# Performance work log

Hardware: AMD Instinct MI355X
Metric: run time of the kernel (lower is better)

The kernel has to match this reference:

```python
import jax, jax.numpy as jnp
import numpy as np

B, D, C = 8192, 1024, 8  # batch, input_size, n_conditions


def setup_inputs() -> dict:
    key = jax.random.key(0)
    k1, k2, k3, k4 = jax.random.split(key, 4)
    x = jax.random.normal(k1, (B, D), dtype=jnp.float32)
    condition_ids = jax.random.randint(k2, (B,), 0, C)  # metadata[batch_key] codes
    # Per-condition Linear(D, D) weights (torch layout: [out, in]) and biases
    W = jax.random.normal(k3, (C, D, D), dtype=jnp.float32) / np.sqrt(D)
    b = jax.random.normal(k4, (C, D), dtype=jnp.float32) * 0.01
    return {"x": x, "condition_ids": condition_ids, "W": W, "b": b}


def reference(x, condition_ids, W, b):
    # Original: for each condition c, zero non-member rows of x, apply
    # Linear_c to the FULL batch, then sum partials. Because Linear is
    # affine, the summed result per row is:
    #   out[i] = W[c_i] @ x[i] + sum_c b_c
    # (each bias b_c is added to EVERY row since the Linear runs on the
    #  full masked batch). We keep the dense per-condition GEMM structure.
    onehot = jax.nn.one_hot(condition_ids, C, dtype=x.dtype)  # [B, C]
    y = jnp.einsum('bi,coi->cbo', x, W)                       # [C, B, D]
    out = jnp.einsum('cbo,bc->bo', y, onehot) + b.sum(axis=0)  # [B, D]
    return out
```

## Files before the change

kernel.cpp:

```cpp
#include <hip/hip_runtime.h>
#include <hip/hip_bf16.h>
#include <cstdint>

#define B_ROWS 8192
#define DIM    1024
#define NC     8
#define NXCD   8
#define SLOTS  16

typedef __bf16 bf16;
typedef __bf16 bf16x4 __attribute__((ext_vector_type(4)));
typedef __bf16 bf16x8 __attribute__((ext_vector_type(8)));
typedef float  f32x4  __attribute__((ext_vector_type(4)));

typedef __attribute__((address_space(3))) void* lds_vp;
typedef const __attribute__((address_space(1))) void* gbl_vp;

__global__ __launch_bounds__(1024) void route_kernel(
    const int* __restrict__ ids, const float* __restrict__ b,
    int* __restrict__ row_list, int* __restrict__ xmeta,
    float* __restrict__ bias_sum) {
    __shared__ int wtot_s[16][NC];
    __shared__ int cnt_s[NC];
    __shared__ int off_s[NC];
    __shared__ int used_s[NXCD];
    __shared__ int novf_s[NC];
    int tid = threadIdx.x, lane = tid & 63, wv = tid >> 6;
    const int per = B_ROWS / 1024;
    int base = tid * per;

    if (tid < NXCD * SLOTS) xmeta[tid * 3 + 2] = 0;

    const int4* idv = (const int4*)(ids + base);
    int4 v0 = idv[0], v1 = idv[1];
    int myid[8] = {v0.x, v0.y, v0.z, v0.w, v1.x, v1.y, v1.z, v1.w};
    unsigned long long p0 = 0, p1 = 0;
#pragma unroll
    for (int q = 0; q < 8; q++) {
        int id = myid[q];
        unsigned long long one = 1ull << ((id & 3) << 4);
        if (id < 4) p0 += one; else p1 += one;
    }
    unsigned long long i0 = p0, i1 = p1;
#pragma unroll
    for (int d = 1; d < 64; d <<= 1) {
        unsigned long long u0 = __shfl_up(i0, d, 64);
        unsigned long long u1 = __shfl_up(i1, d, 64);
        if (lane >= d) { i0 += u0; i1 += u1; }
    }
    unsigned long long e0 = i0 - p0, e1 = i1 - p1;
    unsigned long long t0 = __shfl(i0, 63, 64), t1 = __shfl(i1, 63, 64);
    if (lane == 0) {
#pragma unroll
        for (int c = 0; c < 4; c++) {
            wtot_s[wv][c]     = (int)((t0 >> (c << 4)) & 0xFFFF);
            wtot_s[wv][c + 4] = (int)((t1 >> (c << 4)) & 0xFFFF);
        }
    }
    __syncthreads();
    if (tid < NC) {
        int acc = 0;
        for (int w2 = 0; w2 < 16; w2++) { int t = wtot_s[w2][tid]; wtot_s[w2][tid] = acc; acc += t; }
        cnt_s[tid] = acc;
    }
    __syncthreads();
    if (tid < NC) {
        int acc = 0;
        for (int c2 = 0; c2 < tid; c2++) acc += cnt_s[c2];
        off_s[tid] = acc;
    }
    __syncthreads();
    if (tid < 16 * NC) wtot_s[tid >> 3][tid & 7] += off_s[tid & 7];
    __syncthreads();

    if (tid < NC) {
        int c = tid, n = cnt_s[c];
        int tc = (n + 127) >> 7;
        int prim = tc < SLOTS ? tc : SLOTS;
        for (int t = 0; t < prim; t++) {
            int* e = xmeta + (c * SLOTS + t) * 3;
            int rc = n - t * 128; if (rc > 128) rc = 128;
            e[0] = c; e[1] = off_s[c] + t * 128; e[2] = rc;
        }
        used_s[c] = prim;
        novf_s[c] = tc - prim;
    }
    {
        float s = 0.f;
#pragma unroll
        for (int c = 0; c < NC; c++) s += b[c * DIM + tid];
        bias_sum[tid] = s;
    }
    __syncthreads();

    if (tid == 0) {
        int k = 0;
        for (int c = 0; c < NC; c++) {
            for (int t = 0; t < novf_s[c]; t++) {
                for (;;) {
                    int xx = k >> 4, s = k & (SLOTS - 1); k++;
                    if (s >= used_s[xx]) {
                        int* e = xmeta + (xx * SLOTS + s) * 3;
                        int rc = cnt_s[c] - (SLOTS + t) * 128; if (rc > 128) rc = 128;
                        e[0] = c; e[1] = off_s[c] + (SLOTS + t) * 128; e[2] = rc;
                        break;
                    }
                }
            }
        }
    }
    unsigned long long r0 = 0, r1 = 0;
#pragma unroll
    for (int j = 0; j < per; j++) {
        int id = myid[j];
        int sh = (id & 3) << 4;
        unsigned long long run = (id < 4) ? r0 : r1;
        unsigned long long exc = (id < 4) ? e0 : e1;
        int p = wtot_s[wv][id] + (int)((exc >> sh) & 0xFFFF) + (int)((run >> sh) & 0xFFFF);
        row_list[p] = base + j;
        unsigned long long one = 1ull << sh;
        if (id < 4) r0 += one; else r1 += one;
    }
}

#define XF4 (B_ROWS * DIM / 4)
__global__ __launch_bounds__(1024) void cvt_kernel(
    const float* __restrict__ x, const float* __restrict__ W,
    bf16* __restrict__ xb, bf16* __restrict__ wb) {
    size_t base = (size_t)blockIdx.x * 8192 + threadIdx.x;
    const float4* src;
    bf16* dst;
    if (base < (size_t)XF4) { src = (const float4*)x; dst = xb; }
    else                    { src = (const float4*)W; dst = wb; base -= (size_t)XF4; }
    float4 v[8];
#pragma unroll
    for (int k = 0; k < 8; k++) v[k] = src[base + (size_t)k * 1024];
#pragma unroll
    for (int k = 0; k < 8; k++) {
        bf16x4 o;
        o[0] = (bf16)v[k].x; o[1] = (bf16)v[k].y;
        o[2] = (bf16)v[k].z; o[3] = (bf16)v[k].w;
        *(bf16x4*)(dst + 4 * (base + (size_t)k * 1024)) = o;
    }
}

__global__ __launch_bounds__(256, 2) void gemm_kernel(
    const bf16* __restrict__ xb, const bf16* __restrict__ wb,
    const float* __restrict__ bias_sum, const int* __restrict__ row_list,
    const int* __restrict__ xmeta, float* __restrict__ out) {
    int xcd = blockIdx.x, slot = blockIdx.y, colt = blockIdx.z;
    const int* e = xmeta + (xcd * SLOTS + slot) * 3;
    int cond = e[0], rstart = e[1], rcnt = e[2];
    if (rcnt == 0) return;
    int col0 = colt * 128;

    __shared__ bf16 lds[2][2][128 * 64];

    int tid  = threadIdx.x;
    int lane = tid & 63;
    int w    = tid >> 6;
    int wr   = w >> 1;
    int wc   = w & 1;
    int srow = lane >> 3;
    int scol = ((lane & 7) ^ srow) * 8;

    const bf16 *aS[4], *bS[4];
#pragma unroll
    for (int i = 0; i < 4; i++) {
        int tr = w * 32 + i * 8 + srow;
        int rr = (tr < rcnt) ? tr : 0;
        int grow = row_list[rstart + rr];
        aS[i] = xb + (size_t)grow * DIM + scol;
        bS[i] = wb + (size_t)cond * DIM * DIM + (size_t)(col0 + tr) * DIM + scol;
    }

    f32x4 acc[4][4];
#pragma unroll
    for (int m = 0; m < 4; m++)
#pragma unroll
        for (int n = 0; n < 4; n++) acc[m][n] = (f32x4){0.f, 0.f, 0.f, 0.f};

    int fr = lane & 15;
    int fq = lane >> 4;
    int off0 = (fq * 16) ^ ((fr & 7) << 4);
    int off1 = off0 ^ 64;

    auto stage = [&](int buf, int k0) {
#pragma unroll
        for (int i = 0; i < 4; i++) {
            __builtin_amdgcn_global_load_lds((gbl_vp)(aS[i] + k0),
                                             (lds_vp)(&lds[buf][0][(w * 32 + i * 8) * 64]),
                                             16, 0, 0);
            __builtin_amdgcn_global_load_lds((gbl_vp)(bS[i] + k0),
                                             (lds_vp)(&lds[buf][1][(w * 32 + i * 8) * 64]),
                                             16, 0, 0);
        }
    };

    stage(0, 0);
    stage(1, 64);

    const int NT = DIM / 64;
    for (int t = 0; t < NT; ++t) {
        if (t < NT - 1) asm volatile("s_waitcnt vmcnt(8)" ::: "memory");
        else            asm volatile("s_waitcnt vmcnt(0)" ::: "memory");
        __builtin_amdgcn_s_barrier();

        const char* baseA = (const char*)&lds[t & 1][0][0] + (wr * 64 + fr) * 128;
        const char* baseB = (const char*)&lds[t & 1][1][0] + (wc * 64 + fr) * 128;
#pragma unroll
        for (int kk = 0; kk < 2; ++kk) {
            int ofs = kk ? off1 : off0;
            bf16x8 af[4], bv[4];
#pragma unroll
            for (int m = 0; m < 4; m++) af[m] = *(const bf16x8*)(baseA + m * 2048 + ofs);
#pragma unroll
            for (int n = 0; n < 4; n++) bv[n] = *(const bf16x8*)(baseB + n * 2048 + ofs);
            __builtin_amdgcn_s_setprio(1);
#pragma unroll
            for (int m = 0; m < 4; m++)
#pragma unroll
                for (int n = 0; n < 4; n++)
                    acc[m][n] = __builtin_amdgcn_mfma_f32_16x16x32_bf16(
                        af[m], bv[n], acc[m][n], 0, 0, 0);
            __builtin_amdgcn_s_setprio(0);
        }

        asm volatile("s_waitcnt lgkmcnt(0)" ::: "memory");
        __builtin_amdgcn_s_barrier();
        if (t + 2 < NT) stage(t & 1, (t + 2) * 64);
    }

    float bias[4];
#pragma unroll
    for (int n = 0; n < 4; n++) bias[n] = bias_sum[col0 + wc * 64 + n * 16 + fr];
#pragma unroll
    for (int m = 0; m < 4; m++) {
#pragma unroll
        for (int i = 0; i < 4; i++) {
            int rl = wr * 64 + m * 16 + fq * 4 + i;
            if (rl < rcnt) {
                int grow = row_list[rstart + rl];
                float* op = out + (size_t)grow * DIM + col0 + wc * 64 + fr;
#pragma unroll
                for (int n = 0; n < 4; n++) op[n * 16] = acc[m][n][i] + bias[n];
            }
        }
    }
}

__global__ void naive_kernel(const float* __restrict__ x, const int* __restrict__ ids,
                             const float* __restrict__ W, const float* __restrict__ b,
                             float* __restrict__ out) {
    int row = blockIdx.x;
    int c = ids[row];
    __shared__ float xs[DIM];
    for (int i = threadIdx.x; i < DIM; i += 256) xs[i] = x[(size_t)row * DIM + i];
    __syncthreads();
    const float* Wc = W + (size_t)c * DIM * DIM;
    for (int o = threadIdx.x; o < DIM; o += 256) {
        float s = 0.f;
        const float* wrp = Wc + (size_t)o * DIM;
        for (int i = 0; i < DIM; i++) s += xs[i] * wrp[i];
        float bs = 0.f;
#pragma unroll
        for (int cc = 0; cc < NC; cc++) bs += b[cc * DIM + o];
        out[(size_t)row * DIM + o] = s + bs;
    }
}

extern "C" void kernel_launch(void* const* d_in, const int* in_sizes, int n_in,
                              void* d_out, int out_size, void* d_ws, size_t ws_size,
                              hipStream_t stream) {
    const float* x   = (const float*)d_in[0];
    const int*   ids = (const int*)d_in[1];
    const float* W   = (const float*)d_in[2];
    const float* b   = (const float*)d_in[3];
    float*       out = (float*)d_out;

    size_t xb_off   = 0;
    size_t xb_sz    = (size_t)B_ROWS * DIM * 2;
    size_t wb_off   = (xb_off + xb_sz + 255) & ~(size_t)255;
    size_t wb_sz    = (size_t)NC * DIM * DIM * 2;
    size_t bias_off = (wb_off + wb_sz + 255) & ~(size_t)255;
    size_t rl_off   = (bias_off + DIM * 4 + 255) & ~(size_t)255;
    size_t meta_off = (rl_off + B_ROWS * 4 + 255) & ~(size_t)255;
    size_t need     = meta_off + (size_t)NXCD * SLOTS * 3 * 4;

    if (ws_size < need) {
        naive_kernel<<<dim3(B_ROWS), dim3(256), 0, stream>>>(x, ids, W, b, out);
        return;
    }

    char* ws = (char*)d_ws;
    bf16*  xb       = (bf16*)(ws + xb_off);
    bf16*  wbf      = (bf16*)(ws + wb_off);
    float* bias_sum = (float*)(ws + bias_off);
    int*   row_list = (int*)(ws + rl_off);
    int*   xmeta    = (int*)(ws + meta_off);

    route_kernel<<<dim3(1), dim3(1024), 0, stream>>>(ids, b, row_list, xmeta, bias_sum);
    cvt_kernel<<<dim3(512), dim3(1024), 0, stream>>>(x, W, xb, wbf);
    gemm_kernel<<<dim3(NXCD, SLOTS, 8), dim3(256), 0, stream>>>(xb, wbf, bias_sum,
                                                                row_list, xmeta, out);
}
```

Before: 62.88 us.

## Fuse routing into conversion kernel and widen GEMM tile to 128x256

The single-block routing kernel and the fp32-to-bf16 conversion kernel are merged into one launch, with block 0 doing routing and the other blocks doing conversion. This removes one kernel launch and lets routing overlap with conversion. The GEMM moves to 512-thread blocks with a 128x256 output tile, so each loaded x tile is reused across twice as many output columns and half as many column-tile blocks are launched. The costs are more LDS per block, possibly lower occupancy, and fewer blocks to fill the device.

```diff
diff --git a/kernel.cpp b/kernel.cpp
--- a/kernel.cpp
+++ b/kernel.cpp
@@ -16,10 +16,31 @@
 typedef __attribute__((address_space(3))) void* lds_vp;
 typedef const __attribute__((address_space(1))) void* gbl_vp;
 
-__global__ __launch_bounds__(1024) void route_kernel(
+#define XF4 (B_ROWS * DIM / 4)
+__global__ __launch_bounds__(1024) void prep_kernel(
+    const float* __restrict__ x, const float* __restrict__ W,
     const int* __restrict__ ids, const float* __restrict__ b,
+    bf16* __restrict__ xb, bf16* __restrict__ wb,
     int* __restrict__ row_list, int* __restrict__ xmeta,
     float* __restrict__ bias_sum) {
+    if (blockIdx.x != 0) {
+        size_t base = (size_t)(blockIdx.x - 1) * 8192 + threadIdx.x;
+        const float4* src;
+        bf16* dst;
+        if (base < (size_t)XF4) { src = (const float4*)x; dst = xb; }
+        else                    { src = (const float4*)W; dst = wb; base -= (size_t)XF4; }
+        float4 v[8];
+#pragma unroll
+        for (int k = 0; k < 8; k++) v[k] = src[base + (size_t)k * 1024];
+#pragma unroll
+        for (int k = 0; k < 8; k++) {
+            bf16x4 o;
+            o[0] = (bf16)v[k].x; o[1] = (bf16)v[k].y;
+            o[2] = (bf16)v[k].z; o[3] = (bf16)v[k].w;
+            *(bf16x4*)(dst + 4 * (base + (size_t)k * 1024)) = o;
+        }
+        return;
+    }
     __shared__ int wtot_s[16][NC];
     __shared__ int cnt_s[NC];
     __shared__ int off_s[NC];
@@ -123,28 +144,8 @@
     }
 }
 
-#define XF4 (B_ROWS * DIM / 4)
-__global__ __launch_bounds__(1024) void cvt_kernel(
-    const float* __restrict__ x, const float* __restrict__ W,
-    bf16* __restrict__ xb, bf16* __restrict__ wb) {
-    size_t base = (size_t)blockIdx.x * 8192 + threadIdx.x;
-    const float4* src;
-    bf16* dst;
-    if (base < (size_t)XF4) { src = (const float4*)x; dst = xb; }
-    else                    { src = (const float4*)W; dst = wb; base -= (size_t)XF4; }
-    float4 v[8];
-#pragma unroll
-    for (int k = 0; k < 8; k++) v[k] = src[base + (size_t)k * 1024];
-#pragma unroll
-    for (int k = 0; k < 8; k++) {
-        bf16x4 o;
-        o[0] = (bf16)v[k].x; o[1] = (bf16)v[k].y;
-        o[2] = (bf16)v[k].z; o[3] = (bf16)v[k].w;
-        *(bf16x4*)(dst + 4 * (base + (size_t)k * 1024)) = o;
-    }
-}
-
-__global__ __launch_bounds__(256, 2) void gemm_kernel(
+#define ASZ (128 * 64)
+__global__ __launch_bounds__(512, 2) void gemm_kernel(
     const bf16* __restrict__ xb, const bf16* __restrict__ wb,
     const float* __restrict__ bias_sum, const int* __restrict__ row_list,
     const int* __restrict__ xmeta, float* __restrict__ out) {
@@ -152,26 +153,30 @@
     const int* e = xmeta + (xcd * SLOTS + slot) * 3;
     int cond = e[0], rstart = e[1], rcnt = e[2];
     if (rcnt == 0) return;
-    int col0 = colt * 128;
-
-    __shared__ bf16 lds[2][2][128 * 64];
+    int col0 = colt * 256;
+
+    __shared__ bf16 lds[2][(128 + 256) * 64];
 
     int tid  = threadIdx.x;
     int lane = tid & 63;
     int w    = tid >> 6;
-    int wr   = w >> 1;
-    int wc   = w & 1;
+    int wr   = w >> 2;
+    int wc   = w & 3;
     int srow = lane >> 3;
     int scol = ((lane & 7) ^ srow) * 8;
 
-    const bf16 *aS[4], *bS[4];
-#pragma unroll
-    for (int i = 0; i < 4; i++) {
-        int tr = w * 32 + i * 8 + srow;
+    const bf16 *aS[2], *bS[4];
+#pragma unroll
+    for (int i = 0; i < 2; i++) {
+        int tr = w * 16 + i * 8 + srow;
         int rr = (tr < rcnt) ? tr : 0;
         int grow = row_list[rstart + rr];
         aS[i] = xb + (size_t)grow * DIM + scol;
-        bS[i] = wb + (size_t)cond * DIM * DIM + (size_t)(col0 + tr) * DIM + scol;
+    }
+#pragma unroll
+    for (int i = 0; i < 4; i++) {
+        int br = w * 32 + i * 8 + srow;
+        bS[i] = wb + (size_t)cond * DIM * DIM + (size_t)(col0 + br) * DIM + scol;
     }
 
     f32x4 acc[4][4];
@@ -187,14 +192,15 @@
 
     auto stage = [&](int buf, int k0) {
 #pragma unroll
-        for (int i = 0; i < 4; i++) {
+        for (int i = 0; i < 2; i++)
             __builtin_amdgcn_global_load_lds((gbl_vp)(aS[i] + k0),
-                                             (lds_vp)(&lds[buf][0][(w * 32 + i * 8) * 64]),
+                                             (lds_vp)(&lds[buf][(w * 16 + i * 8) * 64]),
                                              16, 0, 0);
+#pragma unroll
+        for (int i = 0; i < 4; i++)
             __builtin_amdgcn_global_load_lds((gbl_vp)(bS[i] + k0),
-                                             (lds_vp)(&lds[buf][1][(w * 32 + i * 8) * 64]),
+                                             (lds_vp)(&lds[buf][ASZ + (w * 32 + i * 8) * 64]),
                                              16, 0, 0);
-        }
     };
 
     stage(0, 0);
@@ -202,12 +208,12 @@
 
     const int NT = DIM / 64;
     for (int t = 0; t < NT; ++t) {
-        if (t < NT - 1) asm volatile("s_waitcnt vmcnt(8)" ::: "memory");
+        if (t < NT - 1) asm volatile("s_waitcnt vmcnt(6)" ::: "memory");
         else            asm volatile("s_waitcnt vmcnt(0)" ::: "memory");
         __builtin_amdgcn_s_barrier();
 
-        const char* baseA = (const char*)&lds[t & 1][0][0] + (wr * 64 + fr) * 128;
-        const char* baseB = (const char*)&lds[t & 1][1][0] + (wc * 64 + fr) * 128;
+        const char* baseA = (const char*)&lds[t & 1][0] + (wr * 64 + fr) * 128;
+        const char* baseB = (const char*)&lds[t & 1][0] + ASZ * 2 + (wc * 64 + fr) * 128;
 #pragma unroll
         for (int kk = 0; kk < 2; ++kk) {
             int ofs = kk ? off1 : off0;
@@ -299,8 +305,8 @@
     int*   row_list = (int*)(ws + rl_off);
     int*   xmeta    = (int*)(ws + meta_off);
 
-    route_kernel<<<dim3(1), dim3(1024), 0, stream>>>(ids, b, row_list, xmeta, bias_sum);
-    cvt_kernel<<<dim3(512), dim3(1024), 0, stream>>>(x, W, xb, wbf);
-    gemm_kernel<<<dim3(NXCD, SLOTS, 8), dim3(256), 0, stream>>>(xb, wbf, bias_sum,
-                                                                row_list, xmeta, out);
+    prep_kernel<<<dim3(513), dim3(1024), 0, stream>>>(x, W, ids, b, xb, wbf,
+                                                      row_list, xmeta, bias_sum);
+    gemm_kernel<<<dim3(NXCD, SLOTS, DIM / 256), dim3(512), 0, stream>>>(
+        xb, wbf, bias_sum, row_list, xmeta, out);
 }
```

New measurement: 62.90 us. Within noise of the previous version (+0.0%).

## Fuse fp32-to-bf16 conversion into GEMM tile loading, drop cvt kernel

Applied to the files above, without the earlier changes.

Removes the separate conversion kernel that wrote bf16 copies of x and W to workspace. The GEMM now loads fp32 tiles through registers, converts them to bf16 and writes them to swizzled LDS. The next tile's global loads are issued before the MFMA work on the current tile. This saves a full read-write pass and a kernel launch, but each tile now reads twice as many bytes. It also gives up direct global-to-LDS loads and needs more registers, with W and x re-read in fp32 by every block.

```diff
diff --git a/kernel.cpp b/kernel.cpp
--- a/kernel.cpp
+++ b/kernel.cpp
@@ -7,14 +7,13 @@
 #define NC     8
 #define NXCD   8
 #define SLOTS  16
+#define BM     128
+#define BN     128
+#define NT     16
 
 typedef __bf16 bf16;
-typedef __bf16 bf16x4 __attribute__((ext_vector_type(4)));
 typedef __bf16 bf16x8 __attribute__((ext_vector_type(8)));
 typedef float  f32x4  __attribute__((ext_vector_type(4)));
-
-typedef __attribute__((address_space(3))) void* lds_vp;
-typedef const __attribute__((address_space(1))) void* gbl_vp;
 
 __global__ __launch_bounds__(1024) void route_kernel(
     const int* __restrict__ ids, const float* __restrict__ b,
@@ -75,12 +74,12 @@
 
     if (tid < NC) {
         int c = tid, n = cnt_s[c];
-        int tc = (n + 127) >> 7;
+        int tc = (n + BM - 1) >> 7;
         int prim = tc < SLOTS ? tc : SLOTS;
         for (int t = 0; t < prim; t++) {
             int* e = xmeta + (c * SLOTS + t) * 3;
-            int rc = n - t * 128; if (rc > 128) rc = 128;
-            e[0] = c; e[1] = off_s[c] + t * 128; e[2] = rc;
+            int rc = n - t * BM; if (rc > BM) rc = BM;
+            e[0] = c; e[1] = off_s[c] + t * BM; e[2] = rc;
         }
         used_s[c] = prim;
         novf_s[c] = tc - prim;
@@ -101,8 +100,8 @@
                     int xx = k >> 4, s = k & (SLOTS - 1); k++;
                     if (s >= used_s[xx]) {
                         int* e = xmeta + (xx * SLOTS + s) * 3;
-                        int rc = cnt_s[c] - (SLOTS + t) * 128; if (rc > 128) rc = 128;
-                        e[0] = c; e[1] = off_s[c] + (SLOTS + t) * 128; e[2] = rc;
+                        int rc = cnt_s[c] - (SLOTS + t) * BM; if (rc > BM) rc = BM;
+                        e[0] = c; e[1] = off_s[c] + (SLOTS + t) * BM; e[2] = rc;
                         break;
                     }
                 }
@@ -123,38 +122,19 @@
     }
 }
 
-#define XF4 (B_ROWS * DIM / 4)
-__global__ __launch_bounds__(1024) void cvt_kernel(
+#define BUFB 32768
+#define ABYT 16384
+__global__ __launch_bounds__(256, 2) void gemm_kernel(
     const float* __restrict__ x, const float* __restrict__ W,
-    bf16* __restrict__ xb, bf16* __restrict__ wb) {
-    size_t base = (size_t)blockIdx.x * 8192 + threadIdx.x;
-    const float4* src;
-    bf16* dst;
-    if (base < (size_t)XF4) { src = (const float4*)x; dst = xb; }
-    else                    { src = (const float4*)W; dst = wb; base -= (size_t)XF4; }
-    float4 v[8];
-#pragma unroll
-    for (int k = 0; k < 8; k++) v[k] = src[base + (size_t)k * 1024];
-#pragma unroll
-    for (int k = 0; k < 8; k++) {
-        bf16x4 o;
-        o[0] = (bf16)v[k].x; o[1] = (bf16)v[k].y;
-        o[2] = (bf16)v[k].z; o[3] = (bf16)v[k].w;
-        *(bf16x4*)(dst + 4 * (base + (size_t)k * 1024)) = o;
-    }
-}
-
-__global__ __launch_bounds__(256, 2) void gemm_kernel(
-    const bf16* __restrict__ xb, const bf16* __restrict__ wb,
     const float* __restrict__ bias_sum, const int* __restrict__ row_list,
     const int* __restrict__ xmeta, float* __restrict__ out) {
     int xcd = blockIdx.x, slot = blockIdx.y, colt = blockIdx.z;
     const int* e = xmeta + (xcd * SLOTS + slot) * 3;
     int cond = e[0], rstart = e[1], rcnt = e[2];
     if (rcnt == 0) return;
-    int col0 = colt * 128;
-
-    __shared__ bf16 lds[2][2][128 * 64];
+    int col0 = colt * BN;
+
+    __shared__ char lds[2 * BUFB];
 
     int tid  = threadIdx.x;
     int lane = tid & 63;
@@ -162,16 +142,20 @@
     int wr   = w >> 1;
     int wc   = w & 1;
     int srow = lane >> 3;
-    int scol = ((lane & 7) ^ srow) * 8;
-
-    const bf16 *aS[4], *bS[4];
+    int g    = lane & 7;
+
+    const float *aF[4], *bF[4];
+    int wofsA[4], wofsB[4];
 #pragma unroll
     for (int i = 0; i < 4; i++) {
         int tr = w * 32 + i * 8 + srow;
         int rr = (tr < rcnt) ? tr : 0;
         int grow = row_list[rstart + rr];
-        aS[i] = xb + (size_t)grow * DIM + scol;
-        bS[i] = wb + (size_t)cond * DIM * DIM + (size_t)(col0 + tr) * DIM + scol;
+        aF[i] = x + (size_t)grow * DIM + g * 8;
+        wofsA[i] = tr * 128 + ((g ^ srow) * 16);
+        int br = w * 32 + i * 8 + srow;
+        bF[i] = W + (size_t)cond * DIM * DIM + (size_t)(col0 + br) * DIM + g * 8;
+        wofsB[i] = ABYT + br * 128 + ((g ^ srow) * 16);
     }
 
     f32x4 acc[4][4];
@@ -185,37 +169,54 @@
     int off0 = (fq * 16) ^ ((fr & 7) << 4);
     int off1 = off0 ^ 64;
 
-    auto stage = [&](int buf, int k0) {
+    float4 va[4][2], vb[4][2];
+
+    auto LOAD = [&](int k0) {
 #pragma unroll
         for (int i = 0; i < 4; i++) {
-            __builtin_amdgcn_global_load_lds((gbl_vp)(aS[i] + k0),
-                                             (lds_vp)(&lds[buf][0][(w * 32 + i * 8) * 64]),
-                                             16, 0, 0);
-            __builtin_amdgcn_global_load_lds((gbl_vp)(bS[i] + k0),
-                                             (lds_vp)(&lds[buf][1][(w * 32 + i * 8) * 64]),
-                                             16, 0, 0);
+            va[i][0] = *(const float4*)(aF[i] + k0);
+            va[i][1] = *(const float4*)(aF[i] + k0 + 4);
+            vb[i][0] = *(const float4*)(bF[i] + k0);
+            vb[i][1] = *(const float4*)(bF[i] + k0 + 4);
         }
     };
-
-    stage(0, 0);
-    stage(1, 64);
-
-    const int NT = DIM / 64;
+    auto WRITE = [&](int buf) {
+#pragma unroll
+        for (int i = 0; i < 4; i++) {
+            bf16x8 oa, ob;
+            oa[0] = (bf16)va[i][0].x; oa[1] = (bf16)va[i][0].y;
+            oa[2] = (bf16)va[i][0].z; oa[3] = (bf16)va[i][0].w;
+            oa[4] = (bf16)va[i][1].x; oa[5] = (bf16)va[i][1].y;
+            oa[6] = (bf16)va[i][1].z; oa[7] = (bf16)va[i][1].w;
+            ob[0] = (bf16)vb[i][0].x; ob[1] = (bf16)vb[i][0].y;
+            ob[2] = (bf16)vb[i][0].z; ob[3] = (bf16)vb[i][0].w;
+            ob[4] = (bf16)vb[i][1].x; ob[5] = (bf16)vb[i][1].y;
+            ob[6] = (bf16)vb[i][1].z; ob[7] = (bf16)vb[i][1].w;
+            *(bf16x8*)(lds + buf * BUFB + wofsA[i]) = oa;
+            *(bf16x8*)(lds + buf * BUFB + wofsB[i]) = ob;
+        }
+    };
+
+    LOAD(0);
+    WRITE(0);
+    LOAD(64);
+    asm volatile("s_waitcnt lgkmcnt(0)" ::: "memory");
+    __builtin_amdgcn_s_barrier();
+
     for (int t = 0; t < NT; ++t) {
-        if (t < NT - 1) asm volatile("s_waitcnt vmcnt(8)" ::: "memory");
-        else            asm volatile("s_waitcnt vmcnt(0)" ::: "memory");
-        __builtin_amdgcn_s_barrier();
-
-        const char* baseA = (const char*)&lds[t & 1][0][0] + (wr * 64 + fr) * 128;
-        const char* baseB = (const char*)&lds[t & 1][1][0] + (wc * 64 + fr) * 128;
+        if (t + 1 < NT) WRITE((t + 1) & 1);
+        if (t + 2 < NT) LOAD((t + 2) * 64);
+
+        const char* bA = lds + (t & 1) * BUFB + (wr * 64 + fr) * 128;
+        const char* bB = lds + (t & 1) * BUFB + ABYT + (wc * 64 + fr) * 128;
 #pragma unroll
         for (int kk = 0; kk < 2; ++kk) {
             int ofs = kk ? off1 : off0;
             bf16x8 af[4], bv[4];
 #pragma unroll
-            for (int m = 0; m < 4; m++) af[m] = *(const bf16x8*)(baseA + m * 2048 + ofs);
-#pragma unroll
-            for (int n = 0; n < 4; n++) bv[n] = *(const bf16x8*)(baseB + n * 2048 + ofs);
+            for (int m = 0; m < 4; m++) af[m] = *(const bf16x8*)(bA + m * 2048 + ofs);
+#pragma unroll
+            for (int n = 0; n < 4; n++) bv[n] = *(const bf16x8*)(bB + n * 2048 + ofs);
             __builtin_amdgcn_s_setprio(1);
 #pragma unroll
             for (int m = 0; m < 4; m++)
@@ -228,7 +229,6 @@
 
         asm volatile("s_waitcnt lgkmcnt(0)" ::: "memory");
         __builtin_amdgcn_s_barrier();
-        if (t + 2 < NT) stage(t & 1, (t + 2) * 64);
     }
 
     float bias[4];
@@ -278,11 +278,7 @@
     const float* b   = (const float*)d_in[3];
     float*       out = (float*)d_out;
 
-    size_t xb_off   = 0;
-    size_t xb_sz    = (size_t)B_ROWS * DIM * 2;
-    size_t wb_off   = (xb_off + xb_sz + 255) & ~(size_t)255;
-    size_t wb_sz    = (size_t)NC * DIM * DIM * 2;
-    size_t bias_off = (wb_off + wb_sz + 255) & ~(size_t)255;
+    size_t bias_off = 0;
     size_t rl_off   = (bias_off + DIM * 4 + 255) & ~(size_t)255;
     size_t meta_off = (rl_off + B_ROWS * 4 + 255) & ~(size_t)255;
     size_t need     = meta_off + (size_t)NXCD * SLOTS * 3 * 4;
@@ -293,14 +289,11 @@
     }
 
     char* ws = (char*)d_ws;
-    bf16*  xb       = (bf16*)(ws + xb_off);
-    bf16*  wbf      = (bf16*)(ws + wb_off);
     float* bias_sum = (float*)(ws + bias_off);
     int*   row_list = (int*)(ws + rl_off);
     int*   xmeta    = (int*)(ws + meta_off);
 
     route_kernel<<<dim3(1), dim3(1024), 0, stream>>>(ids, b, row_list, xmeta, bias_sum);
-    cvt_kernel<<<dim3(512), dim3(1024), 0, stream>>>(x, W, xb, wbf);
-    gemm_kernel<<<dim3(NXCD, SLOTS, 8), dim3(256), 0, stream>>>(xb, wbf, bias_sum,
-                                                                row_list, xmeta, out);
-}
+    gemm_kernel<<<dim3(NXCD, SLOTS, DIM / BN), dim3(256), 0, stream>>>(
+        x, W, bias_sum, row_list, xmeta, out);
+}
```

After: 66.92 us. +6.4%, slower.

## Fuse routing, bf16 conversion and grouped GEMM into one cooperative persistent kernel

Applied to the files above, without the earlier changes.

Replaces the three launches (route, convert, GEMM) with a single cooperative kernel of 512 blocks. Block 0 does routing and the bias sum while the others convert x and W to bf16, then a grid-wide sync precedes the GEMM, where each block handles two slots. This removes launch gaps and kernel-boundary drains. It relies on all 512 blocks being co-resident, adds the cost of a grid barrier, and puts the routing on a single 256-thread block. A fallback path merges route and convert into one prep kernel followed by the GEMM.

```diff
diff --git a/kernel.cpp b/kernel.cpp
--- a/kernel.cpp
+++ b/kernel.cpp
@@ -1,12 +1,19 @@
 #include <hip/hip_runtime.h>
 #include <hip/hip_bf16.h>
+#include <hip/hip_cooperative_groups.h>
 #include <cstdint>
+
+namespace cg = cooperative_groups;
 
 #define B_ROWS 8192
 #define DIM    1024
 #define NC     8
 #define NXCD   8
 #define SLOTS  16
+#define BM     128
+#define BN     128
+#define NT     16
+#define NBLK   512
 
 typedef __bf16 bf16;
 typedef __bf16 bf16x4 __attribute__((ext_vector_type(4)));
@@ -16,10 +23,282 @@
 typedef __attribute__((address_space(3))) void* lds_vp;
 typedef const __attribute__((address_space(1))) void* gbl_vp;
 
-__global__ __launch_bounds__(1024) void route_kernel(
+#define BUFB 32768
+#define ABYT 16384
+
+__global__ __launch_bounds__(256, 2) void mega_kernel(
+    const float* __restrict__ x, const float* __restrict__ W,
     const int* __restrict__ ids, const float* __restrict__ b,
+    float* __restrict__ out, bf16* __restrict__ xb, bf16* __restrict__ wb,
+    float* __restrict__ bias_sum, int* __restrict__ row_list,
+    int* __restrict__ xmeta) {
+    __shared__ char lds[2 * BUFB];
+
+    int bid = blockIdx.x, tid = threadIdx.x;
+
+    if (bid == 0) {
+        __shared__ int wtot_s[4][NC];
+        __shared__ int cnt_s[NC];
+        __shared__ int off_s[NC];
+        __shared__ int used_s[NXCD];
+        __shared__ int novf_s[NC];
+        int lane = tid & 63, wv = tid >> 6;
+        int base = tid * 32;
+
+        if (tid < NXCD * SLOTS) xmeta[tid * 3 + 2] = 0;
+
+        unsigned long long p0 = 0, p1 = 0;
+        for (int q = 0; q < 4; q++) {
+            const int4* iv = (const int4*)(ids + base + q * 8);
+            int4 v0 = iv[0], v1 = iv[1];
+            int m[8] = {v0.x, v0.y, v0.z, v0.w, v1.x, v1.y, v1.z, v1.w};
+#pragma unroll
+            for (int j = 0; j < 8; j++) {
+                unsigned long long one = 1ull << ((m[j] & 3) << 4);
+                if (m[j] < 4) p0 += one; else p1 += one;
+            }
+        }
+        unsigned long long i0 = p0, i1 = p1;
+#pragma unroll
+        for (int d = 1; d < 64; d <<= 1) {
+            unsigned long long u0 = __shfl_up(i0, d, 64);
+            unsigned long long u1 = __shfl_up(i1, d, 64);
+            if (lane >= d) { i0 += u0; i1 += u1; }
+        }
+        unsigned long long e0 = i0 - p0, e1 = i1 - p1;
+        unsigned long long t0 = __shfl(i0, 63, 64), t1 = __shfl(i1, 63, 64);
+        if (lane == 0) {
+#pragma unroll
+            for (int c = 0; c < 4; c++) {
+                wtot_s[wv][c]     = (int)((t0 >> (c << 4)) & 0xFFFF);
+                wtot_s[wv][c + 4] = (int)((t1 >> (c << 4)) & 0xFFFF);
+            }
+        }
+        __syncthreads();
+        if (tid < NC) {
+            int acc = 0;
+            for (int w2 = 0; w2 < 4; w2++) { int t = wtot_s[w2][tid]; wtot_s[w2][tid] = acc; acc += t; }
+            cnt_s[tid] = acc;
+        }
+        __syncthreads();
+        if (tid < NC) {
+            int acc = 0;
+            for (int c2 = 0; c2 < tid; c2++) acc += cnt_s[c2];
+            off_s[tid] = acc;
+        }
+        __syncthreads();
+        if (tid < 4 * NC) wtot_s[tid >> 3][tid & 7] += off_s[tid & 7];
+        __syncthreads();
+
+        if (tid < NC) {
+            int c = tid, n = cnt_s[c];
+            int tc = (n + BM - 1) >> 7;
+            int prim = tc < SLOTS ? tc : SLOTS;
+            for (int t = 0; t < prim; t++) {
+                int* e = xmeta + (c * SLOTS + t) * 3;
+                int rc = n - t * BM; if (rc > BM) rc = BM;
+                e[0] = c; e[1] = off_s[c] + t * BM; e[2] = rc;
+            }
+            used_s[c] = prim;
+            novf_s[c] = tc - prim;
+        }
+#pragma unroll
+        for (int k = 0; k < DIM / 256; k++) {
+            int d = tid + k * 256;
+            float s = 0.f;
+#pragma unroll
+            for (int c = 0; c < NC; c++) s += b[c * DIM + d];
+            bias_sum[d] = s;
+        }
+        __syncthreads();
+        if (tid == 0) {
+            int k = 0;
+            for (int c = 0; c < NC; c++) {
+                for (int t = 0; t < novf_s[c]; t++) {
+                    for (;;) {
+                        int xx = k >> 4, s = k & (SLOTS - 1); k++;
+                        if (s >= used_s[xx]) {
+                            int* e = xmeta + (xx * SLOTS + s) * 3;
+                            int rc = cnt_s[c] - (SLOTS + t) * BM; if (rc > BM) rc = BM;
+                            e[0] = c; e[1] = off_s[c] + (SLOTS + t) * BM; e[2] = rc;
+                            break;
+                        }
+                    }
+                }
+            }
+        }
+        unsigned long long r0 = 0, r1 = 0;
+        for (int q = 0; q < 4; q++) {
+            const int4* iv = (const int4*)(ids + base + q * 8);
+            int4 v0 = iv[0], v1 = iv[1];
+            int m[8] = {v0.x, v0.y, v0.z, v0.w, v1.x, v1.y, v1.z, v1.w};
+#pragma unroll
+            for (int j = 0; j < 8; j++) {
+                int id = m[j];
+                int sh = (id & 3) << 4;
+                unsigned long long run = (id < 4) ? r0 : r1;
+                unsigned long long exc = (id < 4) ? e0 : e1;
+                int p = wtot_s[wv][id] + (int)((exc >> sh) & 0xFFFF) + (int)((run >> sh) & 0xFFFF);
+                row_list[p] = base + q * 8 + j;
+                unsigned long long one = 1ull << sh;
+                if (id < 4) r0 += one; else r1 += one;
+            }
+        }
+    } else {
+        const size_t XCHK = (size_t)B_ROWS * DIM / 8;
+        for (size_t i = (size_t)(bid - 1) * 256 + tid; i < XCHK; i += 511u * 256u) {
+            const float4* s = (const float4*)x + 2 * i;
+            float4 a = s[0], c4 = s[1];
+            bf16x8 o;
+            o[0] = (bf16)a.x;  o[1] = (bf16)a.y;  o[2] = (bf16)a.z;  o[3] = (bf16)a.w;
+            o[4] = (bf16)c4.x; o[5] = (bf16)c4.y; o[6] = (bf16)c4.z; o[7] = (bf16)c4.w;
+            *(bf16x8*)(xb + 8 * i) = o;
+        }
+        if (bid >= 8) {
+            int c = bid & 7, wi = (bid >> 3) - 1;
+            const size_t WCHK = (size_t)DIM * DIM / 8;
+            const float* Wc = W + (size_t)c * DIM * DIM;
+            bf16* wc = wb + (size_t)c * DIM * DIM;
+            for (size_t i = (size_t)wi * 256 + tid; i < WCHK; i += 63u * 256u) {
+                const float4* s = (const float4*)Wc + 2 * i;
+                float4 a = s[0], c4 = s[1];
+                bf16x8 o;
+                o[0] = (bf16)a.x;  o[1] = (bf16)a.y;  o[2] = (bf16)a.z;  o[3] = (bf16)a.w;
+                o[4] = (bf16)c4.x; o[5] = (bf16)c4.y; o[6] = (bf16)c4.z; o[7] = (bf16)c4.w;
+                *(bf16x8*)(wc + 8 * i) = o;
+            }
+        }
+    }
+
+    cg::this_grid().sync();
+
+    int xcd  = bid & 7;
+    int r    = bid >> 3;
+    int slot = r & 7;
+    int colt = r >> 3;
+    int col0 = colt * BN;
+
+    int lane = tid & 63;
+    int w    = tid >> 6;
+    int wr   = w >> 1;
+    int wc   = w & 1;
+    int srow = lane >> 3;
+    int scol = ((lane & 7) ^ srow) * 8;
+    int fr   = lane & 15;
+    int fq   = lane >> 4;
+    int off0 = (fq * 16) ^ ((fr & 7) << 4);
+    int off1 = off0 ^ 64;
+
+    for (int sp = 0; sp < 2; sp++) {
+        int s2 = slot + sp * 8;
+        const int* e = xmeta + (xcd * SLOTS + s2) * 3;
+        int cond = e[0], rstart = e[1], rcnt = e[2];
+        if (rcnt == 0) continue;
+
+        const bf16 *aS[4], *bS[4];
+#pragma unroll
+        for (int i = 0; i < 4; i++) {
+            int tr = w * 32 + i * 8 + srow;
+            int rr = (tr < rcnt) ? tr : 0;
+            int grow = row_list[rstart + rr];
+            aS[i] = xb + (size_t)grow * DIM + scol;
+            bS[i] = wb + (size_t)cond * DIM * DIM + (size_t)(col0 + tr) * DIM + scol;
+        }
+
+        f32x4 acc[4][4];
+#pragma unroll
+        for (int m = 0; m < 4; m++)
+#pragma unroll
+            for (int n = 0; n < 4; n++) acc[m][n] = (f32x4){0.f, 0.f, 0.f, 0.f};
+
+        auto stage = [&](int buf, int k0) {
+#pragma unroll
+            for (int i = 0; i < 4; i++) {
+                __builtin_amdgcn_global_load_lds((gbl_vp)(aS[i] + k0),
+                    (lds_vp)(lds + buf * BUFB + (w * 32 + i * 8) * 128), 16, 0, 0);
+                __builtin_amdgcn_global_load_lds((gbl_vp)(bS[i] + k0),
+                    (lds_vp)(lds + buf * BUFB + ABYT + (w * 32 + i * 8) * 128), 16, 0, 0);
+            }
+        };
+
+        __syncthreads();
+        stage(0, 0);
+        stage(1, 64);
+
+        for (int t = 0; t < NT; ++t) {
+            if (t < NT - 1) asm volatile("s_waitcnt vmcnt(8)" ::: "memory");
+            else            asm volatile("s_waitcnt vmcnt(0)" ::: "memory");
+            __builtin_amdgcn_s_barrier();
+
+            const char* bA = lds + (t & 1) * BUFB + (wr * 64 + fr) * 128;
+            const char* bB = lds + (t & 1) * BUFB + ABYT + (wc * 64 + fr) * 128;
+#pragma unroll
+            for (int kk = 0; kk < 2; ++kk) {
+                int ofs = kk ? off1 : off0;
+                bf16x8 af[4], bv[4];
+#pragma unroll
+                for (int m = 0; m < 4; m++) af[m] = *(const bf16x8*)(bA + m * 2048 + ofs);
+#pragma unroll
+                for (int n = 0; n < 4; n++) bv[n] = *(const bf16x8*)(bB + n * 2048 + ofs);
+                __builtin_amdgcn_s_setprio(1);
+#pragma unroll
+                for (int m = 0; m < 4; m++)
+#pragma unroll
+                    for (int n = 0; n < 4; n++)
+                        acc[m][n] = __builtin_amdgcn_mfma_f32_16x16x32_bf16(
+                            af[m], bv[n], acc[m][n], 0, 0, 0);
+                __builtin_amdgcn_s_setprio(0);
+            }
+
+            asm volatile("s_waitcnt lgkmcnt(0)" ::: "memory");
+            __builtin_amdgcn_s_barrier();
+            if (t + 2 < NT) stage(t & 1, (t + 2) * 64);
+        }
+
+        float bias[4];
+#pragma unroll
+        for (int n = 0; n < 4; n++) bias[n] = bias_sum[col0 + wc * 64 + n * 16 + fr];
+#pragma unroll
+        for (int m = 0; m < 4; m++) {
+#pragma unroll
+            for (int i = 0; i < 4; i++) {
+                int rl = wr * 64 + m * 16 + fq * 4 + i;
+                if (rl < rcnt) {
+                    int grow = row_list[rstart + rl];
+                    float* op = out + (size_t)grow * DIM + col0 + wc * 64 + fr;
+#pragma unroll
+                    for (int n = 0; n < 4; n++) op[n * 16] = acc[m][n][i] + bias[n];
+                }
+            }
+        }
+    }
+}
+
+#define XF4 (B_ROWS * DIM / 4)
+__global__ __launch_bounds__(1024) void prep_kernel(
+    const float* __restrict__ x, const float* __restrict__ W,
+    const int* __restrict__ ids, const float* __restrict__ b,
+    bf16* __restrict__ xb, bf16* __restrict__ wb,
     int* __restrict__ row_list, int* __restrict__ xmeta,
     float* __restrict__ bias_sum) {
+    if (blockIdx.x != 0) {
+        size_t base = (size_t)(blockIdx.x - 1) * 8192 + threadIdx.x;
+        const float4* src;
+        bf16* dst;
+        if (base < (size_t)XF4) { src = (const float4*)x; dst = xb; }
+        else                    { src = (const float4*)W; dst = wb; base -= (size_t)XF4; }
+        float4 v[8];
+#pragma unroll
+        for (int k = 0; k < 8; k++) v[k] = src[base + (size_t)k * 1024];
+#pragma unroll
+        for (int k = 0; k < 8; k++) {
+            bf16x4 o;
+            o[0] = (bf16)v[k].x; o[1] = (bf16)v[k].y;
+            o[2] = (bf16)v[k].z; o[3] = (bf16)v[k].w;
+            *(bf16x4*)(dst + 4 * (base + (size_t)k * 1024)) = o;
+        }
+        return;
+    }
     __shared__ int wtot_s[16][NC];
     __shared__ int cnt_s[NC];
     __shared__ int off_s[NC];
@@ -75,12 +354,12 @@
 
     if (tid < NC) {
         int c = tid, n = cnt_s[c];
-        int tc = (n + 127) >> 7;
+        int tc = (n + BM - 1) >> 7;
         int prim = tc < SLOTS ? tc : SLOTS;
         for (int t = 0; t < prim; t++) {
             int* e = xmeta + (c * SLOTS + t) * 3;
-            int rc = n - t * 128; if (rc > 128) rc = 128;
-            e[0] = c; e[1] = off_s[c] + t * 128; e[2] = rc;
+            int rc = n - t * BM; if (rc > BM) rc = BM;
+            e[0] = c; e[1] = off_s[c] + t * BM; e[2] = rc;
         }
         used_s[c] = prim;
         novf_s[c] = tc - prim;
@@ -92,7 +371,6 @@
         bias_sum[tid] = s;
     }
     __syncthreads();
-
     if (tid == 0) {
         int k = 0;
         for (int c = 0; c < NC; c++) {
@@ -101,8 +379,8 @@
                     int xx = k >> 4, s = k & (SLOTS - 1); k++;
                     if (s >= used_s[xx]) {
                         int* e = xmeta + (xx * SLOTS + s) * 3;
-                        int rc = cnt_s[c] - (SLOTS + t) * 128; if (rc > 128) rc = 128;
-                        e[0] = c; e[1] = off_s[c] + (SLOTS + t) * 128; e[2] = rc;
+                        int rc = cnt_s[c] - (SLOTS + t) * BM; if (rc > BM) rc = BM;
+                        e[0] = c; e[1] = off_s[c] + (SLOTS + t) * BM; e[2] = rc;
                         break;
                     }
                 }
@@ -123,27 +401,6 @@
     }
 }
 
-#define XF4 (B_ROWS * DIM / 4)
-__global__ __launch_bounds__(1024) void cvt_kernel(
-    const float* __restrict__ x, const float* __restrict__ W,
-    bf16* __restrict__ xb, bf16* __restrict__ wb) {
-    size_t base = (size_t)blockIdx.x * 8192 + threadIdx.x;
-    const float4* src;
-    bf16* dst;
-    if (base < (size_t)XF4) { src = (const float4*)x; dst = xb; }
-    else                    { src = (const float4*)W; dst = wb; base -= (size_t)XF4; }
-    float4 v[8];
-#pragma unroll
-    for (int k = 0; k < 8; k++) v[k] = src[base + (size_t)k * 1024];
-#pragma unroll
-    for (int k = 0; k < 8; k++) {
-        bf16x4 o;
-        o[0] = (bf16)v[k].x; o[1] = (bf16)v[k].y;
-        o[2] = (bf16)v[k].z; o[3] = (bf16)v[k].w;
-        *(bf16x4*)(dst + 4 * (base + (size_t)k * 1024)) = o;
-    }
-}
-
 __global__ __launch_bounds__(256, 2) void gemm_kernel(
     const bf16* __restrict__ xb, const bf16* __restrict__ wb,
     const float* __restrict__ bias_sum, const int* __restrict__ row_list,
@@ -152,9 +409,9 @@
     const int* e = xmeta + (xcd * SLOTS + slot) * 3;
     int cond = e[0], rstart = e[1], rcnt = e[2];
     if (rcnt == 0) return;
-    int col0 = colt * 128;
-
-    __shared__ bf16 lds[2][2][128 * 64];
+    int col0 = colt * BN;
+
+    __shared__ char lds[2 * BUFB];
 
     int tid  = threadIdx.x;
     int lane = tid & 63;
@@ -189,33 +446,30 @@
 #pragma unroll
         for (int i = 0; i < 4; i++) {
             __builtin_amdgcn_global_load_lds((gbl_vp)(aS[i] + k0),
-                                             (lds_vp)(&lds[buf][0][(w * 32 + i * 8) * 64]),
-                                             16, 0, 0);
+                (lds_vp)(lds + buf * BUFB + (w * 32 + i * 8) * 128), 16, 0, 0);
             __builtin_amdgcn_global_load_lds((gbl_vp)(bS[i] + k0),
-                                             (lds_vp)(&lds[buf][1][(w * 32 + i * 8) * 64]),
-                                             16, 0, 0);
+                (lds_vp)(lds + buf * BUFB + ABYT + (w * 32 + i * 8) * 128), 16, 0, 0);
         }
     };
 
     stage(0, 0);
     stage(1, 64);
 
-    const int NT = DIM / 64;
     for (int t = 0; t < NT; ++t) {
         if (t < NT - 1) asm volatile("s_waitcnt vmcnt(8)" ::: "memory");
         else            asm volatile("s_waitcnt vmcnt(0)" ::: "memory");
         __builtin_amdgcn_s_barrier();
 
-        const char* baseA = (const char*)&lds[t & 1][0][0] + (wr * 64 + fr) * 128;
-        const char* baseB = (const char*)&lds[t & 1][1][0] + (wc * 64 + fr) * 128;
+        const char* bA = lds + (t & 1) * BUFB + (wr * 64 + fr) * 128;
+        const char* bB = lds + (t & 1) * BUFB + ABYT + (wc * 64 + fr) * 128;
 #pragma unroll
         for (int kk = 0; kk < 2; ++kk) {
             int ofs = kk ? off1 : off0;
             bf16x8 af[4], bv[4];
 #pragma unroll
-            for (int m = 0; m < 4; m++) af[m] = *(const bf16x8*)(baseA + m * 2048 + ofs);
-#pragma unroll
-            for (int n = 0; n < 4; n++) bv[n] = *(const bf16x8*)(baseB + n * 2048 + ofs);
+            for (int m = 0; m < 4; m++) af[m] = *(const bf16x8*)(bA + m * 2048 + ofs);
+#pragma unroll
+            for (int n = 0; n < 4; n++) bv[n] = *(const bf16x8*)(bB + n * 2048 + ofs);
             __builtin_amdgcn_s_setprio(1);
 #pragma unroll
             for (int m = 0; m < 4; m++)
@@ -299,8 +553,15 @@
     int*   row_list = (int*)(ws + rl_off);
     int*   xmeta    = (int*)(ws + meta_off);
 
-    route_kernel<<<dim3(1), dim3(1024), 0, stream>>>(ids, b, row_list, xmeta, bias_sum);
-    cvt_kernel<<<dim3(512), dim3(1024), 0, stream>>>(x, W, xb, wbf);
-    gemm_kernel<<<dim3(NXCD, SLOTS, 8), dim3(256), 0, stream>>>(xb, wbf, bias_sum,
-                                                                row_list, xmeta, out);
+    void* args[] = {(void*)&x, (void*)&W, (void*)&ids, (void*)&b, (void*)&out,
+                    (void*)&xb, (void*)&wbf, (void*)&bias_sum, (void*)&row_list,
+                    (void*)&xmeta};
+    hipError_t err = hipLaunchCooperativeKernel((const void*)mega_kernel,
+                                                dim3(NBLK), dim3(256), args, 0, stream);
+    if (err == hipSuccess) return;
+
+    prep_kernel<<<dim3(513), dim3(1024), 0, stream>>>(x, W, ids, b, xb, wbf,
+                                                      row_list, xmeta, bias_sum);
+    gemm_kernel<<<dim3(NXCD, SLOTS, DIM / BN), dim3(256), 0, stream>>>(
+        xb, wbf, bias_sum, row_list, xmeta, out);
 }
```

New measurement: 141.5 us. 2.25x slower.
